# Optimization experiments

Hardware: AMD Instinct MI355X
Metric: run time of the kernel (lower is better)

The kernel has to match this reference:

```python
import jax, jax.numpy as jnp
import numpy as np
from jax import lax

MARGIN = 0.5
EPS = 1e-12


def _l2norm(x, axis=-1):
    n = jnp.sqrt(jnp.sum(x * x, axis=axis, keepdims=True))
    return x / jnp.maximum(n, EPS)


def setup_inputs() -> dict:
    key = jax.random.key(0)
    ks = jax.random.split(key, 18)
    B, T, N, Din = 1, 8, 4096, 128
    hid = 256
    D = 2 * hid  # out_dim = 2*hidden_dim[-1]
    Tp, Ttr, M, K = 4, 5, 2048, 16
    s = 0.05
    return {
        "x_feature": jax.random.normal(ks[0], (B, Ttr, N, 1), jnp.float32),
        "x_graph": jax.random.normal(ks[1], (B, T, N, Din), jnp.float32),
        "x_graph_inv": jax.random.normal(ks[2], (B, T, N, Din), jnp.float32),
        "temp_y": jax.random.randint(ks[3], (Tp, M, 2 + K), 0, N),
        "is_leaf": jax.random.uniform(ks[4], (Tp, N), dtype=jnp.float32),
        "W_gcn": jax.random.normal(ks[5], (Din, hid), jnp.float32) * s,
        "b_gcn": jnp.zeros((hid,), jnp.float32),
        "Wx_zr": jax.random.normal(ks[6], (D, 2 * D), jnp.float32) * s,
        "Wh_zr": jax.random.normal(ks[7], (D, 2 * D), jnp.float32) * s,
        "b_zr": jnp.zeros((2 * D,), jnp.float32),
        "Wx_c": jax.random.normal(ks[8], (D, D), jnp.float32) * s,
        "Wh_c": jax.random.normal(ks[9], (D, D), jnp.float32) * s,
        "b_c": jnp.zeros((D,), jnp.float32),
        "h_vecs": jax.random.normal(ks[10], (Tp, D), jnp.float32),
        "W_leaf": jax.random.normal(ks[11], (D, 1), jnp.float32) * s,
        "b_leaf": jnp.zeros((1,), jnp.float32),
        "W_conv": jax.random.normal(ks[12], (Ttr, Tp), jnp.float32) * s,
        "b_conv": jnp.zeros((Tp,), jnp.float32),
        "cur_node_num": N,
    }


def reference(x_feature, x_graph, x_graph_inv, temp_y, is_leaf,
              W_gcn, b_gcn, Wx_zr, Wh_zr, b_zr, Wx_c, Wh_c, b_c,
              h_vecs, W_leaf, b_leaf, W_conv, b_conv, cur_node_num):
    B = x_graph.shape[0]
    N_all = x_graph.shape[2]
    # t_gcn on both graph views, concat -> [B,T,N,D]
    h = jax.nn.relu(jnp.einsum('btnd,dh->btnh', x_graph, W_gcn) + b_gcn)
    h_inv = jax.nn.relu(jnp.einsum('btnd,dh->btnh', x_graph_inv, W_gcn) + b_gcn)
    h_final = jnp.concatenate((h, h_inv), axis=-1)
    D = h_final.shape[-1]

    # sequential GRU (TGCNCell) over time_span via scan
    def cell(hs, x):
        zr = jax.nn.sigmoid(x @ Wx_zr + hs @ Wh_zr + b_zr)
        z, r = jnp.split(zr, 2, axis=-1)
        c = jnp.tanh(x @ Wx_c + (r * hs) @ Wh_c + b_c)
        return z * hs + (1.0 - z) * c, None

    h0 = jnp.zeros((B, N_all, D), h_final.dtype)
    hT, _ = lax.scan(cell, h0, jnp.moveaxis(h_final, 1, 0))
    h_trans = _l2norm(hT.reshape(-1, D)[:cur_node_num])  # [N,D]

    # grid predictions (t_conv surrogate): [B,Ttr,N,1] -> [Tp, B*N] -> [Tp,N]
    feat = x_feature[..., 0].transpose(0, 2, 1)            # [B,N,Ttr]
    g = feat @ W_conv + b_conv                             # [B,N,Tp]
    grid_x = jnp.moveaxis(g, 2, 0).reshape(g.shape[-1], -1)[:, :cur_node_num]

    # Householder reflections per predicted step
    hn = _l2norm(h_vecs)                                   # [Tp,D]
    W_trans = jnp.eye(D, dtype=hn.dtype) - 2.0 * hn[:, :, None] * hn[:, None, :]

    leaf_logits = jax.nn.sigmoid(h_trans @ W_leaf + b_leaf)  # [N,1]
    lvec = leaf_logits[:, 0]

    def per_t(W_t, idx_t, yleaf_t, grid_t):
        pos = h_trans[idx_t[:, 1]]            # [M,D]
        neg = h_trans[idx_t[:, 2:]]           # [M,K,D]
        a = pos @ W_t                          # [M,D]
        score_neg = 1.0 - jnp.einsum('md,mkd->mk', a, neg)
        score_pos = 1.0 - jnp.sum(a * pos, axis=-1, keepdims=True)
        loss_off = jnp.mean(jax.nn.relu(score_pos - score_neg + MARGIN))
        # BCEWithLogits applied to sigmoid outputs (faithful to source)
        loss_leaf = jnp.mean(jnp.maximum(lvec, 0.0) - lvec * yleaf_t + jnp.log1p(jnp.exp(-jnp.abs(lvec))))
        h_s = h_trans @ W_t                    # [N,D]
        score_all = h_s @ h_s.T                # [N,N]
        final = lvec * grid_t                  # [N]
        att = score_all @ final                # [N]
        return att, loss_off, loss_leaf

    att_pre, lo, ll = jax.vmap(per_t)(W_trans, temp_y, is_leaf, grid_x)
    return att_pre, jnp.mean(lo), jnp.mean(ll)
```

## Files before the change

kernel.cpp:

```cpp
#include <hip/hip_runtime.h>
#include <hip/hip_bf16.h>
#include <hip/hip_fp16.h>
#include <math.h>

typedef __hip_bfloat16 bf16;
typedef __attribute__((ext_vector_type(8))) short short8;
typedef __attribute__((ext_vector_type(4))) float f32x4;

union UB { short8 v; bf16 e[8]; };
union UH { short8 v; __half e[8]; };

__device__ __forceinline__ float wred(float v) {
  #pragma unroll
  for (int o = 32; o > 0; o >>= 1) v += __shfl_xor(v, o, 64);
  return v;
}
__device__ __forceinline__ float sigf(float x) { return 1.f / (1.f + expf(-x)); }

__device__ __forceinline__ void gl_lds16(const bf16* g, const bf16* lds) {
  __builtin_amdgcn_global_load_lds((const __attribute__((address_space(1))) void*)g,
                                   (__attribute__((address_space(3))) void*)lds,
                                   16, 0, 0);
}
__device__ __forceinline__ f32x4 mfma16(short8 a, short8 b, f32x4 c) {
  return __builtin_amdgcn_mfma_f32_16x16x32_bf16(a, b, c, 0, 0, 0);
}

__global__ __launch_bounds__(256, 2)
void gemmx(const bf16* __restrict__ A, const bf16* __restrict__ Wxzrt,
           const bf16* __restrict__ Wxct, const float* __restrict__ b_zr,
           const float* __restrict__ b_c, bf16* __restrict__ xzrp,
           bf16* __restrict__ xcp)
{
  __shared__ __align__(16) char smem[34816];
  bf16* As = (bf16*)smem;
  bf16* Bs = (bf16*)(smem + 16384);
  __half* Ts = (__half*)smem;

  const int tid  = threadIdx.x;
  const int wave = tid >> 6, lane = tid & 63;
  const int lm = lane & 15, q = lane >> 4;
  const int brow = blockIdx.x, bcol = blockIdx.y;
  const int wr = (wave >> 1) * 64, wc = (wave & 1) * 64;
  const int srow = lane >> 3, sslot = lane & 7;

  const bf16* Bt; const float* bias; bf16* C; int ldc, colbase;
  if (bcol < 8) { Bt = Wxzrt + (size_t)bcol * 128 * 512; bias = b_zr; C = xzrp; ldc = 1024; colbase = bcol * 128; }
  else          { Bt = Wxct + (size_t)(bcol - 8) * 128 * 512; bias = b_c; C = xcp; ldc = 512; colbase = (bcol - 8) * 128; }

  f32x4 acc[4][4];
  #pragma unroll
  for (int i = 0; i < 4; ++i)
    #pragma unroll
    for (int j = 0; j < 4; ++j) acc[i][j] = (f32x4){0.f, 0.f, 0.f, 0.f};

  for (int kb = 0; kb < 512; kb += 64) {
    #pragma unroll
    for (int j = 0; j < 4; ++j) {
      int ml = wave * 32 + j * 8 + srow;
      int cg = sslot ^ (ml & 7);
      gl_lds16(A + (size_t)(brow * 128 + ml) * 512 + kb + cg * 8, As + (wave * 4 + j) * 512);
      gl_lds16(Bt + (size_t)ml * 512 + kb + cg * 8, Bs + (wave * 4 + j) * 512);
    }
    __syncthreads();
    #pragma unroll
    for (int ks = 0; ks < 2; ++ks) {
      short8 af[4], bfr[4];
      #pragma unroll
      for (int i = 0; i < 4; ++i) {
        int cg = ks * 4 + q;
        int ml = wr + i * 16 + lm;
        af[i]  = *(const short8*)(As + ml * 64 + ((cg ^ (ml & 7)) * 8));
        int nl = wc + i * 16 + lm;
        bfr[i] = *(const short8*)(Bs + nl * 64 + ((cg ^ (nl & 7)) * 8));
      }
      #pragma unroll
      for (int i = 0; i < 4; ++i)
        #pragma unroll
        for (int j = 0; j < 4; ++j)
          acc[i][j] = mfma16(af[i], bfr[j], acc[i][j]);
    }
    __syncthreads();
  }
  #pragma unroll
  for (int i = 0; i < 4; ++i)
    #pragma unroll
    for (int j = 0; j < 4; ++j) {
      int col = wc + j * 16 + lm;
      float bv = bias[colbase + col];
      #pragma unroll
      for (int p = 0; p < 4; ++p)
        Ts[(wr + i * 16 + q * 4 + p) * 136 + col] = __float2half(acc[i][j][p] + bv);
    }
  __syncthreads();
  int rg = tid >> 4, cl = tid & 15;
  #pragma unroll
  for (int v = 0; v < 8; ++v) {
    int row = v * 16 + rg;
    UH t; t.v = *(const short8*)(Ts + row * 136 + cl * 8);
    UB o;
    #pragma unroll
    for (int e = 0; e < 8; ++e) o.e[e] = __float2bfloat16(__half2float(t.e[e]));
    *(short8*)(C + (size_t)(brow * 128 + row) * ldc + colbase + cl * 8) = o.v;
  }
}

__global__ __launch_bounds__(256, 2)
void gcnk(const float* __restrict__ Ag, const float* __restrict__ Agi,
          const bf16* __restrict__ Wgt, const float* __restrict__ bias,
          bf16* __restrict__ out)
{
  __shared__ __align__(16) char smem[34816];
  bf16* As = (bf16*)smem;
  bf16* Bs = (bf16*)(smem + 16384);
  __half* Ts = (__half*)smem;

  const int tid  = threadIdx.x;
  const int wave = tid >> 6, lane = tid & 63;
  const int lm = lane & 15, q = lane >> 4;
  const int brow = blockIdx.x, bcol = blockIdx.y;
  const int z = blockIdx.z, cout = z * 256;
  const float* A = z ? Agi : Ag;
  const int wr = (wave >> 1) * 64, wc = (wave & 1) * 64;
  const int srow = lane >> 3, sslot = lane & 7;

  f32x4 acc[4][4];
  #pragma unroll
  for (int i = 0; i < 4; ++i)
    #pragma unroll
    for (int j = 0; j < 4; ++j) acc[i][j] = (f32x4){0.f, 0.f, 0.f, 0.f};

  for (int kb = 0; kb < 128; kb += 64) {
    #pragma unroll
    for (int j = 0; j < 4; ++j) {
      int ml = wave * 32 + j * 8 + srow;
      int cg = sslot ^ (ml & 7);
      const float* src = A + (size_t)(brow * 128 + ml) * 128 + kb + cg * 8;
      bf16 tmp[8];
      #pragma unroll
      for (int e = 0; e < 8; ++e) tmp[e] = __float2bfloat16(src[e]);
      *(short8*)(As + ml * 64 + sslot * 8) = *(const short8*)tmp;
      gl_lds16(Wgt + (size_t)(bcol * 128 + ml) * 128 + kb + cg * 8,
               Bs + (wave * 4 + j) * 512);
    }
    __syncthreads();
    #pragma unroll
    for (int ks = 0; ks < 2; ++ks) {
      short8 af[4], bfr[4];
      #pragma unroll
      for (int i = 0; i < 4; ++i) {
        int cg = ks * 4 + q;
        int ml = wr + i * 16 + lm;
        af[i]  = *(const short8*)(As + ml * 64 + ((cg ^ (ml & 7)) * 8));
        int nl = wc + i * 16 + lm;
        bfr[i] = *(const short8*)(Bs + nl * 64 + ((cg ^ (nl & 7)) * 8));
      }
      #pragma unroll
      for (int i = 0; i < 4; ++i)
        #pragma unroll
        for (int j = 0; j < 4; ++j)
          acc[i][j] = mfma16(af[i], bfr[j], acc[i][j]);
    }
    __syncthreads();
  }
  #pragma unroll
  for (int i = 0; i < 4; ++i)
    #pragma unroll
    for (int j = 0; j < 4; ++j) {
      int col = wc + j * 16 + lm;
      float bv = bias[bcol * 128 + col];
      #pragma unroll
      for (int p = 0; p < 4; ++p)
        Ts[(wr + i * 16 + q * 4 + p) * 136 + col] = __float2half(acc[i][j][p] + bv);
    }
  __syncthreads();
  int rg = tid >> 4, cl = tid & 15;
  #pragma unroll
  for (int v = 0; v < 8; ++v) {
    int row = v * 16 + rg;
    UH t; t.v = *(const short8*)(Ts + row * 136 + cl * 8);
    UB o;
    #pragma unroll
    for (int e = 0; e < 8; ++e) o.e[e] = __float2bfloat16(fmaxf(__half2float(t.e[e]), 0.f));
    *(short8*)(out + (size_t)(brow * 128 + row) * 512 + cout + bcol * 128 + cl * 8) = o.v;
  }
}

__global__ __launch_bounds__(256, 2)
void gruk(const bf16* __restrict__ A, const bf16* __restrict__ Bt,
          const bf16* __restrict__ xpre, int ldx, int mode,
          __half* __restrict__ zh, bf16* __restrict__ rhb,
          bf16* __restrict__ hsb)
{
  __shared__ __align__(16) char smem[32768];
  bf16* As = (bf16*)smem;
  bf16* Bs = (bf16*)(smem + 16384);
  __half* Ts = (__half*)smem;

  const int tid  = threadIdx.x;
  const int wave = tid >> 6, lane = tid & 63;
  const int lm = lane & 15, q = lane >> 4;
  const int brow = blockIdx.x, bcol = blockIdx.y;
  const int srow4 = lane >> 4, sslot = lane & 15;

  f32x4 acc[4];
  #pragma unroll
  for (int j = 0; j < 4; ++j) acc[j] = (f32x4){0.f, 0.f, 0.f, 0.f};

  for (int kb = 0; kb < 512; kb += 128) {
    #pragma unroll
    for (int c = 0; c < 4; ++c) {
      int r = wave * 16 + c * 4 + srow4;
      int cg = sslot ^ (r & 15);
      gl_lds16(A + (size_t)(brow * 64 + r) * 512 + kb + cg * 8,
               As + (wave * 16 + c * 4) * 128);
      gl_lds16(Bt + (size_t)(bcol * 64 + r) * 512 + kb + cg * 8,
               Bs + (wave * 16 + c * 4) * 128);
    }
    __syncthreads();
    #pragma unroll
    for (int ks = 0; ks < 4; ++ks) {
      int cg = ks * 4 + q;
      int ar = wave * 16 + lm;
      short8 af = *(const short8*)(As + ar * 128 + ((cg ^ (ar & 15)) * 8));
      #pragma unroll
      for (int j = 0; j < 4; ++j) {
        int nr = j * 16 + lm;
        short8 b8 = *(const short8*)(Bs + nr * 128 + ((cg ^ (nr & 15)) * 8));
        acc[j] = mfma16(af, b8, acc[j]);
      }
    }
    __syncthreads();
  }
  #pragma unroll
  for (int j = 0; j < 4; ++j)
    #pragma unroll
    for (int p = 0; p < 4; ++p)
      Ts[(wave * 16 + q * 4 + p) * 72 + j * 16 + lm] = __float2half(acc[j][p]);
  __syncthreads();
  int rg = tid >> 3, cl = tid & 7;
  #pragma unroll
  for (int v = 0; v < 2; ++v) {
    int row = v * 32 + rg;
    int lcol = cl * 8;
    int gcol = bcol * 64 + lcol;
    size_t grow = (size_t)(brow * 64 + row);
    UH t; t.v = *(const short8*)(Ts + row * 72 + lcol);
    UB xv; xv.v = *(const short8*)(xpre + grow * ldx + gcol);
    if (mode == 1) {
      if (bcol < 8) {
        UH o;
        #pragma unroll
        for (int e = 0; e < 8; ++e)
          o.e[e] = __float2half(sigf(__half2float(t.e[e]) + (float)xv.e[e]));
        *(short8*)(zh + grow * 512 + gcol) = o.v;
      } else {
        int rc = gcol - 512;
        UB h8; h8.v = *(const short8*)(hsb + grow * 512 + rc);
        UB o;
        #pragma unroll
        for (int e = 0; e < 8; ++e) {
          float s = sigf(__half2float(t.e[e]) + (float)xv.e[e]);
          o.e[e] = __float2bfloat16(s * (float)h8.e[e]);
        }
        *(short8*)(rhb + grow * 512 + rc) = o.v;
      }
    } else {
      UB h8; h8.v = *(const short8*)(hsb + grow * 512 + gcol);
      UH z8; z8.v = *(const short8*)(zh + grow * 512 + gcol);
      UB o;
      #pragma unroll
      for (int e = 0; e < 8; ++e) {
        float c = tanhf(__half2float(t.e[e]) + (float)xv.e[e]);
        float zc = __half2float(z8.e[e]);
        o.e[e] = __float2bfloat16(zc * (float)h8.e[e] + (1.f - zc) * c);
      }
      *(short8*)(hsb + grow * 512 + gcol) = o.v;
    }
  }
}

__global__ void prep(const float* __restrict__ Wh_zr, const float* __restrict__ Wh_c,
                     const float* __restrict__ Wx_zr, const float* __restrict__ Wx_c,
                     const float* __restrict__ W_gcn,
                     bf16* __restrict__ Whzrt, bf16* __restrict__ Whct,
                     bf16* __restrict__ Wxzrt, bf16* __restrict__ Wxct,
                     bf16* __restrict__ Wgt) {
  int i = blockIdx.x * 256 + threadIdx.x;
  if (i < 524288) {
    int n = i >> 9, k = i & 511;
    Whzrt[i] = __float2bfloat16(Wh_zr[(size_t)k * 1024 + n]);
  } else if (i < 786432) {
    int j = i - 524288; int n = j >> 9, k = j & 511;
    Whct[j] = __float2bfloat16(Wh_c[(size_t)k * 512 + n]);
  } else if (i < 1310720) {
    int j = i - 786432; int n = j >> 9, k = j & 511;
    Wxzrt[j] = __float2bfloat16(Wx_zr[(size_t)k * 1024 + n]);
  } else if (i < 1572864) {
    int j = i - 1310720; int n = j >> 9, k = j & 511;
    Wxct[j] = __float2bfloat16(Wx_c[(size_t)k * 512 + n]);
  } else {
    int j = i - 1572864; int n = j >> 7, k = j & 127;
    Wgt[j] = __float2bfloat16(W_gcn[(size_t)k * 256 + n]);
  }
}

__global__ void norm_lvec(const bf16* __restrict__ hsb, const float* __restrict__ Wl,
                          const float* __restrict__ bl, const float* __restrict__ hv,
                          bf16* __restrict__ Htrb, float* __restrict__ lv,
                          float* __restrict__ hn) {
  int w = threadIdx.x >> 6, lane = threadIdx.x & 63;
  if (blockIdx.x == 1024) {
    float x[8], ss = 0.f;
    #pragma unroll
    for (int j = 0; j < 8; ++j) { x[j] = hv[w * 512 + lane * 8 + j]; ss += x[j] * x[j]; }
    ss = wred(ss);
    float inv = 1.f / fmaxf(sqrtf(ss), 1e-12f);
    #pragma unroll
    for (int j = 0; j < 8; ++j) hn[w * 512 + lane * 8 + j] = x[j] * inv;
    return;
  }
  int n = blockIdx.x * 4 + w;
  float x[8], ss = 0.f;
  #pragma unroll
  for (int j = 0; j < 8; ++j) {
    x[j] = (float)hsb[(size_t)n * 512 + lane * 8 + j];
    ss += x[j] * x[j];
  }
  ss = wred(ss);
  float inv = 1.f / fmaxf(sqrtf(ss), 1e-12f);
  float dot = 0.f;
  #pragma unroll
  for (int j = 0; j < 8; ++j) {
    float vv = x[j] * inv;
    Htrb[(size_t)n * 512 + lane * 8 + j] = __float2bfloat16(vv);
    dot += vv * Wl[lane * 8 + j];
  }
  dot = wred(dot);
  if (lane == 0) lv[n] = sigf(dot + bl[0]);
}

__global__ void htf(const bf16* __restrict__ Htrb, const float* __restrict__ xf,
                    const float* __restrict__ Wc, const float* __restrict__ bc,
                    const float* __restrict__ lv, float* __restrict__ v) {
  __shared__ float fin_s[4][64];
  int ch = blockIdx.x;
  int d = threadIdx.x;
  int n0 = ch * 64;
  if (d < 256) {
    int t = d >> 6, i = d & 63, n = n0 + i;
    float g = bc[t];
    #pragma unroll
    for (int tt = 0; tt < 5; ++tt) g += xf[tt * 4096 + n] * Wc[tt * 4 + t];
    fin_s[t][i] = lv[n] * g;
  }
  __syncthreads();
  float s0 = 0.f, s1 = 0.f, s2 = 0.f, s3 = 0.f;
  for (int i = 0; i < 64; ++i) {
    float hv = (float)Htrb[(size_t)(n0 + i) * 512 + d];
    s0 += hv * fin_s[0][i];
    s1 += hv * fin_s[1][i];
    s2 += hv * fin_s[2][i];
    s3 += hv * fin_s[3][i];
  }
  atomicAdd(&v[d], s0);
  atomicAdd(&v[512 + d], s1);
  atomicAdd(&v[1024 + d], s2);
  atomicAdd(&v[1536 + d], s3);
}

__global__ void attk(const bf16* __restrict__ Htrb, const float* __restrict__ v,
                     float* __restrict__ out) {
  int w = threadIdx.x >> 6, lane = threadIdx.x & 63;
  int n = blockIdx.x * 4 + w;
  float x[8];
  #pragma unroll
  for (int j = 0; j < 8; ++j) x[j] = (float)Htrb[(size_t)n * 512 + lane * 8 + j];
  #pragma unroll
  for (int t = 0; t < 4; ++t) {
    float s = 0.f;
    #pragma unroll
    for (int j = 0; j < 8; ++j) s += x[j] * v[t * 512 + lane * 8 + j];
    s = wred(s);
    if (lane == 0) out[t * 4096 + n] = s;
  }
}

__global__ void loff(const bf16* __restrict__ Htrb, const float* __restrict__ hn,
                     const int* __restrict__ ty, float* __restrict__ loffp) {
  int w = threadIdx.x >> 6, lane = threadIdx.x & 63;
  int t = blockIdx.y;
  int m = blockIdx.x * 4 + w;
  const int* row = ty + ((size_t)t * 2048 + m) * 18;
  int pi = row[1];
  float p[8], hv[8], c = 0.f;
  #pragma unroll
  for (int j = 0; j < 8; ++j) {
    p[j]  = (float)Htrb[(size_t)pi * 512 + lane * 8 + j];
    hv[j] = hn[t * 512 + lane * 8 + j];
    c += p[j] * hv[j];
  }
  c = wred(c);
  float a[8], sp = 0.f;
  #pragma unroll
  for (int j = 0; j < 8; ++j) { a[j] = p[j] - 2.f * c * hv[j]; sp += a[j] * p[j]; }
  sp = wred(sp);
  float acc = 0.f;
  for (int k = 0; k < 16; ++k) {
    int ni = row[2 + k];
    float sn = 0.f;
    #pragma unroll
    for (int j = 0; j < 8; ++j) sn += a[j] * (float)Htrb[(size_t)ni * 512 + lane * 8 + j];
    sn = wred(sn);
    acc += fmaxf(sn - sp + 0.5f, 0.f);
  }
  __shared__ float sbuf[4];
  if (lane == 0) sbuf[w] = acc;
  __syncthreads();
  if (threadIdx.x == 0)
    loffp[t * 512 + blockIdx.x] = sbuf[0] + sbuf[1] + sbuf[2] + sbuf[3];
}

__global__ void fini(const float* __restrict__ loffp, const float* __restrict__ lv,
                     const float* __restrict__ yl, float* __restrict__ out) {
  int tid = threadIdx.x, w = tid >> 6, lane = tid & 63;
  float s = 0.f, s2 = 0.f;
  for (int i = tid; i < 2048; i += 256) s += loffp[i];
  for (int i = tid; i < 4096; i += 256) {
    float l = lv[i];
    float ym = 0.25f * (yl[i] + yl[4096 + i] + yl[8192 + i] + yl[12288 + i]);
    s2 += fmaxf(l, 0.f) - l * ym + log1pf(expf(-fabsf(l)));
  }
  s = wred(s); s2 = wred(s2);
  __shared__ float sb[4], sb2[4];
  if (lane == 0) { sb[w] = s; sb2[w] = s2; }
  __syncthreads();
  if (tid == 0) {
    out[16384] = (sb[0] + sb[1] + sb[2] + sb[3]) / (4.f * 2048.f * 16.f);
    out[16385] = (sb2[0] + sb2[1] + sb2[2] + sb2[3]) / 4096.f;
  }
}

__global__ void wsprobe(float marker, float* out) {
  if (threadIdx.x == 0) out[0] = marker;
}

extern "C" void kernel_launch(void* const* d_in, const int* in_sizes, int n_in,
                              void* d_out, int out_size, void* d_ws, size_t ws_size,
                              hipStream_t stream) {
  const float* x_feature   = (const float*)d_in[0];
  const float* x_graph     = (const float*)d_in[1];
  const float* x_graph_inv = (const float*)d_in[2];
  const int*   temp_y      = (const int*)d_in[3];
  const float* is_leaf     = (const float*)d_in[4];
  const float* W_gcn       = (const float*)d_in[5];
  const float* b_gcn       = (const float*)d_in[6];
  const float* Wx_zr       = (const float*)d_in[7];
  const float* Wh_zr       = (const float*)d_in[8];
  const float* b_zr        = (const float*)d_in[9];
  const float* Wx_c        = (const float*)d_in[10];
  const float* Wh_c        = (const float*)d_in[11];
  const float* b_c         = (const float*)d_in[12];
  const float* h_vecs      = (const float*)d_in[13];
  const float* W_leaf      = (const float*)d_in[14];
  const float* b_leaf      = (const float*)d_in[15];
  const float* W_conv      = (const float*)d_in[16];
  const float* b_conv      = (const float*)d_in[17];
  float* out = (float*)d_out;
  (void)in_sizes; (void)n_in; (void)out_size;

  const size_t NEED = 156000000;
  if (ws_size < NEED) {
    wsprobe<<<1, 64, 0, stream>>>(1000.f + (float)(ws_size >> 20), out);
    return;
  }

  char* ws = (char*)d_ws;
  size_t off = 0;
  auto alloc = [&](size_t bytes) -> void* {
    void* p = ws + off;
    off = (off + bytes + 255) & ~(size_t)255;
    return p;
  };
  bf16*   Whzrt = (bf16*)  alloc((size_t)1024 * 512 * 2);
  bf16*   Whct  = (bf16*)  alloc((size_t)512 * 512 * 2);
  bf16*   Wxzrt = (bf16*)  alloc((size_t)1024 * 512 * 2);
  bf16*   Wxct  = (bf16*)  alloc((size_t)512 * 512 * 2);
  bf16*   Wgt   = (bf16*)  alloc((size_t)256 * 128 * 2);
  bf16*   hfin  = (bf16*)  alloc((size_t)32768 * 512 * 2);
  bf16*   xzrp  = (bf16*)  alloc((size_t)32768 * 1024 * 2);
  bf16*   xcp   = (bf16*)  alloc((size_t)32768 * 512 * 2);
  bf16*   hsb   = (bf16*)  alloc((size_t)4096 * 512 * 2);
  bf16*   rhb   = (bf16*)  alloc((size_t)4096 * 512 * 2);
  __half* zh    = (__half*)alloc((size_t)4096 * 512 * 2);
  float*  lv    = (float*) alloc(4096 * 4);
  float*  hn    = (float*) alloc(4 * 512 * 4);
  float*  v     = (float*) alloc(4 * 512 * 4);
  float*  loffp = (float*) alloc(2048 * 4);
  bf16*   Htrb  = hfin;

  hipMemsetAsync(hsb, 0, (size_t)4096 * 512 * 2, stream);
  hipMemsetAsync(v, 0, 4 * 512 * 4, stream);

  prep<<<6272, 256, 0, stream>>>(Wh_zr, Wh_c, Wx_zr, Wx_c, W_gcn,
                                 Whzrt, Whct, Wxzrt, Wxct, Wgt);
  gcnk<<<dim3(256, 2, 2), 256, 0, stream>>>(x_graph, x_graph_inv, Wgt, b_gcn, hfin);
  gemmx<<<dim3(256, 12), 256, 0, stream>>>(hfin, Wxzrt, Wxct, b_zr, b_c, xzrp, xcp);

  for (int t = 0; t < 8; ++t) {
    const bf16* xz = xzrp + (size_t)t * 4096 * 1024;
    const bf16* xc = xcp + (size_t)t * 4096 * 512;
    gruk<<<dim3(64, 16), 256, 0, stream>>>(hsb, Whzrt, xz, 1024, 1, zh, rhb, hsb);
    gruk<<<dim3(64, 8), 256, 0, stream>>>(rhb, Whct, xc, 512, 2, zh, nullptr, hsb);
  }

  norm_lvec<<<1025, 256, 0, stream>>>(hsb, W_leaf, b_leaf, h_vecs, Htrb, lv, hn);
  htf<<<64, 512, 0, stream>>>(Htrb, x_feature, W_conv, b_conv, lv, v);
  attk<<<1024, 256, 0, stream>>>(Htrb, v, out);
  loff<<<dim3(512, 4), 256, 0, stream>>>(Htrb, hn, temp_y, loffp);
  fini<<<1, 256, 0, stream>>>(loffp, lv, is_leaf, out);
}
```

Baseline: 416.3 us.

## Fuse all GRU timesteps into one persistent kernel with LDS-resident state

Replaces the 16 per-timestep GRU GEMM launches with a single kernel in which each block owns 32 rows and keeps the hidden state, r*h and z in LDS across all 8 steps. Recurrent weights are pre-packed into an MFMA-fragment layout so each lane reads B operands directly from global memory without LDS staging. The first step's GEMM is skipped because the hidden state starts at zero, which also removes the initial memset. This cuts launch overhead and global round-trips for the intermediates, at the cost of only 128 blocks on the device, so fewer CUs are busy, and each block rereads the full weight matrices from L2 every step.

```diff
diff --git a/kernel.cpp b/kernel.cpp
--- a/kernel.cpp
+++ b/kernel.cpp
@@ -186,96 +186,170 @@
   }
 }
 
-__global__ __launch_bounds__(256, 2)
-void gruk(const bf16* __restrict__ A, const bf16* __restrict__ Bt,
-          const bf16* __restrict__ xpre, int ldx, int mode,
-          __half* __restrict__ zh, bf16* __restrict__ rhb,
-          bf16* __restrict__ hsb)
+__global__ __launch_bounds__(256, 1)
+void grufuse(const bf16* __restrict__ Wzr, const bf16* __restrict__ Wc,
+             const bf16* __restrict__ xzrp, const bf16* __restrict__ xcp,
+             bf16* __restrict__ hsb)
 {
-  __shared__ __align__(16) char smem[32768];
-  bf16* As = (bf16*)smem;
-  bf16* Bs = (bf16*)(smem + 16384);
-  __half* Ts = (__half*)smem;
+  __shared__ __align__(16) bf16   hls[32 * 512];
+  __shared__ __align__(16) bf16   rls[32 * 512];
+  __shared__ __align__(16) __half zls[32 * 512];
+  __shared__ __align__(16) __half Ts[32 * 136];
 
   const int tid  = threadIdx.x;
   const int wave = tid >> 6, lane = tid & 63;
   const int lm = lane & 15, q = lane >> 4;
-  const int brow = blockIdx.x, bcol = blockIdx.y;
-  const int srow4 = lane >> 4, sslot = lane & 15;
-
-  f32x4 acc[4];
-  #pragma unroll
-  for (int j = 0; j < 4; ++j) acc[j] = (f32x4){0.f, 0.f, 0.f, 0.f};
-
-  for (int kb = 0; kb < 512; kb += 128) {
-    #pragma unroll
-    for (int c = 0; c < 4; ++c) {
-      int r = wave * 16 + c * 4 + srow4;
-      int cg = sslot ^ (r & 15);
-      gl_lds16(A + (size_t)(brow * 64 + r) * 512 + kb + cg * 8,
-               As + (wave * 16 + c * 4) * 128);
-      gl_lds16(Bt + (size_t)(bcol * 64 + r) * 512 + kb + cg * 8,
-               Bs + (wave * 16 + c * 4) * 128);
-    }
-    __syncthreads();
-    #pragma unroll
-    for (int ks = 0; ks < 4; ++ks) {
-      int cg = ks * 4 + q;
-      int ar = wave * 16 + lm;
-      short8 af = *(const short8*)(As + ar * 128 + ((cg ^ (ar & 15)) * 8));
-      #pragma unroll
-      for (int j = 0; j < 4; ++j) {
-        int nr = j * 16 + lm;
-        short8 b8 = *(const short8*)(Bs + nr * 128 + ((cg ^ (nr & 15)) * 8));
-        acc[j] = mfma16(af, b8, acc[j]);
+  const int n0 = blockIdx.x * 32;
+  const int prow = tid >> 3, pcs = (tid & 7) * 16;
+
+  {
+    short8 zz = (short8){0,0,0,0,0,0,0,0};
+    #pragma unroll
+    for (int i = 0; i < 16; ++i)
+      *(short8*)(hls + tid * 128 + i * 8) = zz;
+  }
+  __syncthreads();
+
+  for (int t = 0; t < 8; ++t) {
+    const bf16* xz = xzrp + (size_t)(t * 4096 + n0) * 1024;
+    const bf16* xc = xcp  + (size_t)(t * 4096 + n0) * 512;
+
+    for (int NB = 0; NB < 8; ++NB) {
+      UB xv0, xv1;
+      xv0.v = *(const short8*)(xz + (size_t)prow * 1024 + NB * 128 + pcs);
+      xv1.v = *(const short8*)(xz + (size_t)prow * 1024 + NB * 128 + pcs + 8);
+
+      f32x4 acc[2][2];
+      #pragma unroll
+      for (int i = 0; i < 2; ++i)
+        #pragma unroll
+        for (int j = 0; j < 2; ++j) acc[i][j] = (f32x4){0.f, 0.f, 0.f, 0.f};
+
+      if (t) {
+        const int nb0 = NB * 8 + wave * 2;
+        const bf16* B0 = Wzr + (size_t)(nb0 * 16) * 512 + lane * 8;
+        const bf16* B1 = Wzr + (size_t)((nb0 + 1) * 16) * 512 + lane * 8;
+        #pragma unroll
+        for (int KS = 0; KS < 16; ++KS) {
+          const int s = (((KS * 4 + q) ^ (lm & 7)) * 8);
+          short8 a0 = *(const short8*)(hls + lm * 512 + s);
+          short8 a1 = *(const short8*)(hls + (16 + lm) * 512 + s);
+          short8 b0 = *(const short8*)(B0 + KS * 512);
+          short8 b1 = *(const short8*)(B1 + KS * 512);
+          acc[0][0] = mfma16(a0, b0, acc[0][0]);
+          acc[1][0] = mfma16(a1, b0, acc[1][0]);
+          acc[0][1] = mfma16(a0, b1, acc[0][1]);
+          acc[1][1] = mfma16(a1, b1, acc[1][1]);
+        }
       }
-    }
-    __syncthreads();
-  }
-  #pragma unroll
-  for (int j = 0; j < 4; ++j)
-    #pragma unroll
-    for (int p = 0; p < 4; ++p)
-      Ts[(wave * 16 + q * 4 + p) * 72 + j * 16 + lm] = __float2half(acc[j][p]);
-  __syncthreads();
-  int rg = tid >> 3, cl = tid & 7;
-  #pragma unroll
-  for (int v = 0; v < 2; ++v) {
-    int row = v * 32 + rg;
-    int lcol = cl * 8;
-    int gcol = bcol * 64 + lcol;
-    size_t grow = (size_t)(brow * 64 + row);
-    UH t; t.v = *(const short8*)(Ts + row * 72 + lcol);
-    UB xv; xv.v = *(const short8*)(xpre + grow * ldx + gcol);
-    if (mode == 1) {
-      if (bcol < 8) {
-        UH o;
-        #pragma unroll
-        for (int e = 0; e < 8; ++e)
-          o.e[e] = __float2half(sigf(__half2float(t.e[e]) + (float)xv.e[e]));
-        *(short8*)(zh + grow * 512 + gcol) = o.v;
-      } else {
-        int rc = gcol - 512;
-        UB h8; h8.v = *(const short8*)(hsb + grow * 512 + rc);
-        UB o;
+      #pragma unroll
+      for (int rf = 0; rf < 2; ++rf)
+        #pragma unroll
+        for (int nf = 0; nf < 2; ++nf)
+          #pragma unroll
+          for (int p = 0; p < 4; ++p)
+            Ts[(rf * 16 + q * 4 + p) * 136 + wave * 32 + nf * 16 + lm] =
+              __float2half(acc[rf][nf][p]);
+      __syncthreads();
+      {
+        UH t0, t1;
+        t0.v = *(const short8*)(Ts + prow * 136 + pcs);
+        t1.v = *(const short8*)(Ts + prow * 136 + pcs + 8);
+        if (NB < 4) {
+          int zc = NB * 128 + pcs;
+          UH o0, o1;
+          #pragma unroll
+          for (int e = 0; e < 8; ++e) {
+            o0.e[e] = __float2half(sigf(__half2float(t0.e[e]) + (float)xv0.e[e]));
+            o1.e[e] = __float2half(sigf(__half2float(t1.e[e]) + (float)xv1.e[e]));
+          }
+          *(short8*)(zls + prow * 512 + ((((zc >> 3)    ) ^ (prow & 7)) << 3)) = o0.v;
+          *(short8*)(zls + prow * 512 + ((((zc >> 3) + 1) ^ (prow & 7)) << 3)) = o1.v;
+        } else {
+          int rc = NB * 128 + pcs - 512;
+          UB h0, h1, o0, o1;
+          h0.v = *(const short8*)(hls + prow * 512 + ((((rc >> 3)    ) ^ (prow & 7)) << 3));
+          h1.v = *(const short8*)(hls + prow * 512 + ((((rc >> 3) + 1) ^ (prow & 7)) << 3));
+          #pragma unroll
+          for (int e = 0; e < 8; ++e) {
+            float r0 = sigf(__half2float(t0.e[e]) + (float)xv0.e[e]);
+            float r1 = sigf(__half2float(t1.e[e]) + (float)xv1.e[e]);
+            o0.e[e] = __float2bfloat16(r0 * (float)h0.e[e]);
+            o1.e[e] = __float2bfloat16(r1 * (float)h1.e[e]);
+          }
+          *(short8*)(rls + prow * 512 + ((((rc >> 3)    ) ^ (prow & 7)) << 3)) = o0.v;
+          *(short8*)(rls + prow * 512 + ((((rc >> 3) + 1) ^ (prow & 7)) << 3)) = o1.v;
+        }
+      }
+      __syncthreads();
+    }
+
+    for (int NB = 0; NB < 4; ++NB) {
+      UB xv0, xv1;
+      xv0.v = *(const short8*)(xc + (size_t)prow * 512 + NB * 128 + pcs);
+      xv1.v = *(const short8*)(xc + (size_t)prow * 512 + NB * 128 + pcs + 8);
+
+      f32x4 acc[2][2];
+      #pragma unroll
+      for (int i = 0; i < 2; ++i)
+        #pragma unroll
+        for (int j = 0; j < 2; ++j) acc[i][j] = (f32x4){0.f, 0.f, 0.f, 0.f};
+
+      if (t) {
+        const int nb0 = NB * 8 + wave * 2;
+        const bf16* B0 = Wc + (size_t)(nb0 * 16) * 512 + lane * 8;
+        const bf16* B1 = Wc + (size_t)((nb0 + 1) * 16) * 512 + lane * 8;
+        #pragma unroll
+        for (int KS = 0; KS < 16; ++KS) {
+          const int s = (((KS * 4 + q) ^ (lm & 7)) * 8);
+          short8 a0 = *(const short8*)(rls + lm * 512 + s);
+          short8 a1 = *(const short8*)(rls + (16 + lm) * 512 + s);
+          short8 b0 = *(const short8*)(B0 + KS * 512);
+          short8 b1 = *(const short8*)(B1 + KS * 512);
+          acc[0][0] = mfma16(a0, b0, acc[0][0]);
+          acc[1][0] = mfma16(a1, b0, acc[1][0]);
+          acc[0][1] = mfma16(a0, b1, acc[0][1]);
+          acc[1][1] = mfma16(a1, b1, acc[1][1]);
+        }
+      }
+      #pragma unroll
+      for (int rf = 0; rf < 2; ++rf)
+        #pragma unroll
+        for (int nf = 0; nf < 2; ++nf)
+          #pragma unroll
+          for (int p = 0; p < 4; ++p)
+            Ts[(rf * 16 + q * 4 + p) * 136 + wave * 32 + nf * 16 + lm] =
+              __float2half(acc[rf][nf][p]);
+      __syncthreads();
+      {
+        int col = NB * 128 + pcs;
+        int s0 = (((col >> 3)    ) ^ (prow & 7)) << 3;
+        int s1 = (((col >> 3) + 1) ^ (prow & 7)) << 3;
+        UH t0, t1, z0, z1;
+        t0.v = *(const short8*)(Ts + prow * 136 + pcs);
+        t1.v = *(const short8*)(Ts + prow * 136 + pcs + 8);
+        z0.v = *(const short8*)(zls + prow * 512 + s0);
+        z1.v = *(const short8*)(zls + prow * 512 + s1);
+        UB h0, h1, o0, o1;
+        h0.v = *(const short8*)(hls + prow * 512 + s0);
+        h1.v = *(const short8*)(hls + prow * 512 + s1);
         #pragma unroll
         for (int e = 0; e < 8; ++e) {
-          float s = sigf(__half2float(t.e[e]) + (float)xv.e[e]);
-          o.e[e] = __float2bfloat16(s * (float)h8.e[e]);
+          float c0 = tanhf(__half2float(t0.e[e]) + (float)xv0.e[e]);
+          float c1 = tanhf(__half2float(t1.e[e]) + (float)xv1.e[e]);
+          float za = __half2float(z0.e[e]);
+          float zb = __half2float(z1.e[e]);
+          o0.e[e] = __float2bfloat16(za * (float)h0.e[e] + (1.f - za) * c0);
+          o1.e[e] = __float2bfloat16(zb * (float)h1.e[e] + (1.f - zb) * c1);
         }
-        *(short8*)(rhb + grow * 512 + rc) = o.v;
+        *(short8*)(hls + prow * 512 + s0) = o0.v;
+        *(short8*)(hls + prow * 512 + s1) = o1.v;
+        if (t == 7) {
+          *(short8*)(hsb + (size_t)(n0 + prow) * 512 + col)     = o0.v;
+          *(short8*)(hsb + (size_t)(n0 + prow) * 512 + col + 8) = o1.v;
+        }
       }
-    } else {
-      UB h8; h8.v = *(const short8*)(hsb + grow * 512 + gcol);
-      UH z8; z8.v = *(const short8*)(zh + grow * 512 + gcol);
-      UB o;
-      #pragma unroll
-      for (int e = 0; e < 8; ++e) {
-        float c = tanhf(__half2float(t.e[e]) + (float)xv.e[e]);
-        float zc = __half2float(z8.e[e]);
-        o.e[e] = __float2bfloat16(zc * (float)h8.e[e] + (1.f - zc) * c);
-      }
-      *(short8*)(hsb + grow * 512 + gcol) = o.v;
+      __syncthreads();
     }
   }
 }
@@ -289,10 +363,12 @@
   int i = blockIdx.x * 256 + threadIdx.x;
   if (i < 524288) {
     int n = i >> 9, k = i & 511;
-    Whzrt[i] = __float2bfloat16(Wh_zr[(size_t)k * 1024 + n]);
+    int off = ((n >> 4) * 16 + (k >> 5)) * 512 + ((k >> 3) & 3) * 128 + (n & 15) * 8 + (k & 7);
+    Whzrt[off] = __float2bfloat16(Wh_zr[(size_t)k * 1024 + n]);
   } else if (i < 786432) {
     int j = i - 524288; int n = j >> 9, k = j & 511;
-    Whct[j] = __float2bfloat16(Wh_c[(size_t)k * 512 + n]);
+    int off = ((n >> 4) * 16 + (k >> 5)) * 512 + ((k >> 3) & 3) * 128 + (n & 15) * 8 + (k & 7);
+    Whct[off] = __float2bfloat16(Wh_c[(size_t)k * 512 + n]);
   } else if (i < 1310720) {
     int j = i - 786432; int n = j >> 9, k = j & 511;
     Wxzrt[j] = __float2bfloat16(Wx_zr[(size_t)k * 1024 + n]);
@@ -491,15 +567,12 @@
   bf16*   xzrp  = (bf16*)  alloc((size_t)32768 * 1024 * 2);
   bf16*   xcp   = (bf16*)  alloc((size_t)32768 * 512 * 2);
   bf16*   hsb   = (bf16*)  alloc((size_t)4096 * 512 * 2);
-  bf16*   rhb   = (bf16*)  alloc((size_t)4096 * 512 * 2);
-  __half* zh    = (__half*)alloc((size_t)4096 * 512 * 2);
   float*  lv    = (float*) alloc(4096 * 4);
   float*  hn    = (float*) alloc(4 * 512 * 4);
   float*  v     = (float*) alloc(4 * 512 * 4);
   float*  loffp = (float*) alloc(2048 * 4);
   bf16*   Htrb  = hfin;
 
-  hipMemsetAsync(hsb, 0, (size_t)4096 * 512 * 2, stream);
   hipMemsetAsync(v, 0, 4 * 512 * 4, stream);
 
   prep<<<6272, 256, 0, stream>>>(Wh_zr, Wh_c, Wx_zr, Wx_c, W_gcn,
@@ -507,12 +580,7 @@
   gcnk<<<dim3(256, 2, 2), 256, 0, stream>>>(x_graph, x_graph_inv, Wgt, b_gcn, hfin);
   gemmx<<<dim3(256, 12), 256, 0, stream>>>(hfin, Wxzrt, Wxct, b_zr, b_c, xzrp, xcp);
 
-  for (int t = 0; t < 8; ++t) {
-    const bf16* xz = xzrp + (size_t)t * 4096 * 1024;
-    const bf16* xc = xcp + (size_t)t * 4096 * 512;
-    gruk<<<dim3(64, 16), 256, 0, stream>>>(hsb, Whzrt, xz, 1024, 1, zh, rhb, hsb);
-    gruk<<<dim3(64, 8), 256, 0, stream>>>(rhb, Whct, xc, 512, 2, zh, nullptr, hsb);
-  }
+  grufuse<<<128, 256, 0, stream>>>(Whzrt, Whct, xzrp, xcp, hsb);
 
   norm_lvec<<<1025, 256, 0, stream>>>(hsb, W_leaf, b_leaf, h_vecs, Htrb, lv, hn);
   htf<<<64, 512, 0, stream>>>(Htrb, x_feature, W_conv, b_conv, lv, v);
```

After: 687.0 us. 1.65x slower.

## Restructure GRU step kernels: full-K A tile in LDS, fragment-packed weights from global

Applied to the files above, without the earlier changes.

The generic gruk kernel is replaced by two specialized kernels, gruz and gruc. Each block loads the whole 64x512 row tile of the hidden state into LDS once and streams the recurrent weights straight from global memory into registers. The weights are repacked in prep into an MFMA-fragment-friendly layout so each lane reads them contiguously. Each block now computes a wider output slab (256 or 128 columns) with 4x4 or 4x2 MFMA tiles, giving fewer blocks (256 per launch). The first timestep skips the recurrent GEMM and the hidden-state memset, since h is zero. The trade-offs are lower occupancy (launch bounds 1, 64KB LDS), fewer blocks to fill the GPU, and weight reads from global memory with no LDS reuse.

```diff
diff --git a/kernel.cpp b/kernel.cpp
--- a/kernel.cpp
+++ b/kernel.cpp
@@ -186,97 +186,174 @@
   }
 }
 
-__global__ __launch_bounds__(256, 2)
-void gruk(const bf16* __restrict__ A, const bf16* __restrict__ Bt,
-          const bf16* __restrict__ xpre, int ldx, int mode,
-          __half* __restrict__ zh, bf16* __restrict__ rhb,
-          bf16* __restrict__ hsb)
+__global__ __launch_bounds__(256, 1)
+void gruz(const bf16* __restrict__ hsb, const bf16* __restrict__ Wzr,
+          const bf16* __restrict__ xz, __half* __restrict__ zh,
+          bf16* __restrict__ rhb, int t0)
 {
-  __shared__ __align__(16) char smem[32768];
-  bf16* As = (bf16*)smem;
-  bf16* Bs = (bf16*)(smem + 16384);
-  __half* Ts = (__half*)smem;
+  __shared__ __align__(16) bf16 As[64 * 512];
+  __half* Ts = (__half*)As;
 
   const int tid  = threadIdx.x;
-  const int wave = tid >> 6, lane = tid & 63;
-  const int lm = lane & 15, q = lane >> 4;
-  const int brow = blockIdx.x, bcol = blockIdx.y;
-  const int srow4 = lane >> 4, sslot = lane & 15;
-
-  f32x4 acc[4];
-  #pragma unroll
-  for (int j = 0; j < 4; ++j) acc[j] = (f32x4){0.f, 0.f, 0.f, 0.f};
-
-  for (int kb = 0; kb < 512; kb += 128) {
-    #pragma unroll
-    for (int c = 0; c < 4; ++c) {
-      int r = wave * 16 + c * 4 + srow4;
-      int cg = sslot ^ (r & 15);
-      gl_lds16(A + (size_t)(brow * 64 + r) * 512 + kb + cg * 8,
-               As + (wave * 16 + c * 4) * 128);
-      gl_lds16(Bt + (size_t)(bcol * 64 + r) * 512 + kb + cg * 8,
-               Bs + (wave * 16 + c * 4) * 128);
-    }
-    __syncthreads();
-    #pragma unroll
-    for (int ks = 0; ks < 4; ++ks) {
-      int cg = ks * 4 + q;
-      int ar = wave * 16 + lm;
-      short8 af = *(const short8*)(As + ar * 128 + ((cg ^ (ar & 15)) * 8));
-      #pragma unroll
-      for (int j = 0; j < 4; ++j) {
-        int nr = j * 16 + lm;
-        short8 b8 = *(const short8*)(Bs + nr * 128 + ((cg ^ (nr & 15)) * 8));
-        acc[j] = mfma16(af, b8, acc[j]);
+  const int w    = tid >> 6, lane = tid & 63;
+  const int lm   = lane & 15, q = lane >> 4;
+  const int g    = blockIdx.x, s = blockIdx.y;
+  const int grow = g * 64;
+
+  f32x4 acc[4][4];
+  #pragma unroll
+  for (int mf = 0; mf < 4; ++mf)
+    #pragma unroll
+    for (int nf = 0; nf < 4; ++nf) acc[mf][nf] = (f32x4){0.f, 0.f, 0.f, 0.f};
+
+  if (!t0) {
+    #pragma unroll
+    for (int j = 0; j < 16; ++j) {
+      int row = w * 16 + j;
+      gl_lds16(hsb + (size_t)(grow + row) * 512 + ((lane ^ (row & 7)) * 8),
+               As + row * 512);
+    }
+    __syncthreads();
+    const bf16* Bp = Wzr + (size_t)(s * 16 + w * 4) * 8192 + lane * 8;
+    #pragma unroll
+    for (int KS = 0; KS < 16; ++KS) {
+      short8 a[4];
+      #pragma unroll
+      for (int mf = 0; mf < 4; ++mf) {
+        int row = mf * 16 + lm;
+        a[mf] = *(const short8*)(As + row * 512 + (((KS * 4 + q) ^ (row & 7)) * 8));
       }
-    }
-    __syncthreads();
-  }
-  #pragma unroll
-  for (int j = 0; j < 4; ++j)
-    #pragma unroll
-    for (int p = 0; p < 4; ++p)
-      Ts[(wave * 16 + q * 4 + p) * 72 + j * 16 + lm] = __float2half(acc[j][p]);
+      #pragma unroll
+      for (int nf = 0; nf < 4; ++nf) {
+        short8 b = *(const short8*)(Bp + (size_t)nf * 8192 + KS * 512);
+        #pragma unroll
+        for (int mf = 0; mf < 4; ++mf)
+          acc[mf][nf] = mfma16(a[mf], b, acc[mf][nf]);
+      }
+    }
+    __syncthreads();
+  }
+
+  #pragma unroll
+  for (int mf = 0; mf < 4; ++mf)
+    #pragma unroll
+    for (int nf = 0; nf < 4; ++nf)
+      #pragma unroll
+      for (int p = 0; p < 4; ++p)
+        Ts[(mf * 16 + q * 4 + p) * 264 + w * 64 + nf * 16 + lm] =
+          __float2half(acc[mf][nf][p]);
   __syncthreads();
-  int rg = tid >> 3, cl = tid & 7;
-  #pragma unroll
-  for (int v = 0; v < 2; ++v) {
-    int row = v * 32 + rg;
-    int lcol = cl * 8;
-    int gcol = bcol * 64 + lcol;
-    size_t grow = (size_t)(brow * 64 + row);
-    UH t; t.v = *(const short8*)(Ts + row * 72 + lcol);
-    UB xv; xv.v = *(const short8*)(xpre + grow * ldx + gcol);
-    if (mode == 1) {
-      if (bcol < 8) {
-        UH o;
+
+  const int row = tid >> 2, c0 = (tid & 3) * 64;
+  const size_t gr = (size_t)(grow + row);
+  #pragma unroll
+  for (int j = 0; j < 8; ++j) {
+    int c = c0 + j * 8;
+    UH tv; tv.v = *(const short8*)(Ts + row * 264 + c);
+    UB xv; xv.v = *(const short8*)(xz + gr * 1024 + s * 256 + c);
+    if (s < 2) {
+      UH o;
+      #pragma unroll
+      for (int e = 0; e < 8; ++e)
+        o.e[e] = __float2half(sigf(__half2float(tv.e[e]) + (float)xv.e[e]));
+      *(short8*)(zh + gr * 512 + s * 256 + c) = o.v;
+    } else {
+      int rcol = (s - 2) * 256 + c;
+      UB o;
+      if (t0) {
         #pragma unroll
-        for (int e = 0; e < 8; ++e)
-          o.e[e] = __float2half(sigf(__half2float(t.e[e]) + (float)xv.e[e]));
-        *(short8*)(zh + grow * 512 + gcol) = o.v;
+        for (int e = 0; e < 8; ++e) o.e[e] = __float2bfloat16(0.f);
       } else {
-        int rc = gcol - 512;
-        UB h8; h8.v = *(const short8*)(hsb + grow * 512 + rc);
-        UB o;
+        UB h8; h8.v = *(const short8*)(hsb + gr * 512 + rcol);
         #pragma unroll
         for (int e = 0; e < 8; ++e) {
-          float s = sigf(__half2float(t.e[e]) + (float)xv.e[e]);
-          o.e[e] = __float2bfloat16(s * (float)h8.e[e]);
+          float r = sigf(__half2float(tv.e[e]) + (float)xv.e[e]);
+          o.e[e] = __float2bfloat16(r * (float)h8.e[e]);
         }
-        *(short8*)(rhb + grow * 512 + rc) = o.v;
       }
-    } else {
-      UB h8; h8.v = *(const short8*)(hsb + grow * 512 + gcol);
-      UH z8; z8.v = *(const short8*)(zh + grow * 512 + gcol);
-      UB o;
-      #pragma unroll
-      for (int e = 0; e < 8; ++e) {
-        float c = tanhf(__half2float(t.e[e]) + (float)xv.e[e]);
-        float zc = __half2float(z8.e[e]);
-        o.e[e] = __float2bfloat16(zc * (float)h8.e[e] + (1.f - zc) * c);
+      *(short8*)(rhb + gr * 512 + rcol) = o.v;
+    }
+  }
+}
+
+__global__ __launch_bounds__(256, 1)
+void gruc(const bf16* __restrict__ rhb, const bf16* __restrict__ Wc,
+          const bf16* __restrict__ xc, const __half* __restrict__ zh,
+          bf16* __restrict__ hsb, int t0)
+{
+  __shared__ __align__(16) bf16 As[64 * 512];
+  __half* Ts = (__half*)As;
+
+  const int tid  = threadIdx.x;
+  const int w    = tid >> 6, lane = tid & 63;
+  const int lm   = lane & 15, q = lane >> 4;
+  const int g    = blockIdx.x, s = blockIdx.y;
+  const int grow = g * 64;
+
+  f32x4 acc[4][2];
+  #pragma unroll
+  for (int mf = 0; mf < 4; ++mf)
+    #pragma unroll
+    for (int nf = 0; nf < 2; ++nf) acc[mf][nf] = (f32x4){0.f, 0.f, 0.f, 0.f};
+
+  if (!t0) {
+    #pragma unroll
+    for (int j = 0; j < 16; ++j) {
+      int row = w * 16 + j;
+      gl_lds16(rhb + (size_t)(grow + row) * 512 + ((lane ^ (row & 7)) * 8),
+               As + row * 512);
+    }
+    __syncthreads();
+    const bf16* Bp = Wc + (size_t)(s * 8 + w * 2) * 8192 + lane * 8;
+    #pragma unroll
+    for (int KS = 0; KS < 16; ++KS) {
+      short8 a[4];
+      #pragma unroll
+      for (int mf = 0; mf < 4; ++mf) {
+        int row = mf * 16 + lm;
+        a[mf] = *(const short8*)(As + row * 512 + (((KS * 4 + q) ^ (row & 7)) * 8));
       }
-      *(short8*)(hsb + grow * 512 + gcol) = o.v;
-    }
+      #pragma unroll
+      for (int nf = 0; nf < 2; ++nf) {
+        short8 b = *(const short8*)(Bp + (size_t)nf * 8192 + KS * 512);
+        #pragma unroll
+        for (int mf = 0; mf < 4; ++mf)
+          acc[mf][nf] = mfma16(a[mf], b, acc[mf][nf]);
+      }
+    }
+    __syncthreads();
+  }
+
+  #pragma unroll
+  for (int mf = 0; mf < 4; ++mf)
+    #pragma unroll
+    for (int nf = 0; nf < 2; ++nf)
+      #pragma unroll
+      for (int p = 0; p < 4; ++p)
+        Ts[(mf * 16 + q * 4 + p) * 136 + w * 32 + nf * 16 + lm] =
+          __float2half(acc[mf][nf][p]);
+  __syncthreads();
+
+  const int row = tid >> 2, c0 = (tid & 3) * 32;
+  const size_t gr = (size_t)(grow + row);
+  #pragma unroll
+  for (int j = 0; j < 4; ++j) {
+    int c = c0 + j * 8;
+    int hc = s * 128 + c;
+    UH tv; tv.v = *(const short8*)(Ts + row * 136 + c);
+    UB xv; xv.v = *(const short8*)(xc + gr * 512 + hc);
+    UH zv; zv.v = *(const short8*)(zh + gr * 512 + hc);
+    UB h8;
+    if (!t0) h8.v = *(const short8*)(hsb + gr * 512 + hc);
+    UB o;
+    #pragma unroll
+    for (int e = 0; e < 8; ++e) {
+      float cd = tanhf(__half2float(tv.e[e]) + (float)xv.e[e]);
+      float zc = __half2float(zv.e[e]);
+      float ho = t0 ? 0.f : (float)h8.e[e];
+      o.e[e] = __float2bfloat16(zc * ho + (1.f - zc) * cd);
+    }
+    *(short8*)(hsb + gr * 512 + hc) = o.v;
   }
 }
 
@@ -289,10 +366,12 @@
   int i = blockIdx.x * 256 + threadIdx.x;
   if (i < 524288) {
     int n = i >> 9, k = i & 511;
-    Whzrt[i] = __float2bfloat16(Wh_zr[(size_t)k * 1024 + n]);
+    int off = ((n >> 4) * 16 + (k >> 5)) * 512 + ((k >> 3) & 3) * 128 + (n & 15) * 8 + (k & 7);
+    Whzrt[off] = __float2bfloat16(Wh_zr[(size_t)k * 1024 + n]);
   } else if (i < 786432) {
     int j = i - 524288; int n = j >> 9, k = j & 511;
-    Whct[j] = __float2bfloat16(Wh_c[(size_t)k * 512 + n]);
+    int off = ((n >> 4) * 16 + (k >> 5)) * 512 + ((k >> 3) & 3) * 128 + (n & 15) * 8 + (k & 7);
+    Whct[off] = __float2bfloat16(Wh_c[(size_t)k * 512 + n]);
   } else if (i < 1310720) {
     int j = i - 786432; int n = j >> 9, k = j & 511;
     Wxzrt[j] = __float2bfloat16(Wx_zr[(size_t)k * 1024 + n]);
@@ -499,7 +578,6 @@
   float*  loffp = (float*) alloc(2048 * 4);
   bf16*   Htrb  = hfin;
 
-  hipMemsetAsync(hsb, 0, (size_t)4096 * 512 * 2, stream);
   hipMemsetAsync(v, 0, 4 * 512 * 4, stream);
 
   prep<<<6272, 256, 0, stream>>>(Wh_zr, Wh_c, Wx_zr, Wx_c, W_gcn,
@@ -508,10 +586,12 @@
   gemmx<<<dim3(256, 12), 256, 0, stream>>>(hfin, Wxzrt, Wxct, b_zr, b_c, xzrp, xcp);
 
   for (int t = 0; t < 8; ++t) {
-    const bf16* xz = xzrp + (size_t)t * 4096 * 1024;
-    const bf16* xc = xcp + (size_t)t * 4096 * 512;
-    gruk<<<dim3(64, 16), 256, 0, stream>>>(hsb, Whzrt, xz, 1024, 1, zh, rhb, hsb);
-    gruk<<<dim3(64, 8), 256, 0, stream>>>(rhb, Whct, xc, 512, 2, zh, nullptr, hsb);
+    gruz<<<dim3(64, 4), 256, 0, stream>>>(hsb, Whzrt,
+                                          xzrp + (size_t)t * 4096 * 1024,
+                                          zh, rhb, t == 0);
+    gruc<<<dim3(64, 4), 256, 0, stream>>>(rhb, Whct,
+                                          xcp + (size_t)t * 4096 * 512,
+                                          zh, hsb, t == 0);
   }
 
   norm_lvec<<<1025, 256, 0, stream>>>(hsb, W_leaf, b_leaf, h_vecs, Htrb, lv, hn);
```

New measurement: 520.7 us. 25.1% more time.
